# Kernel tuning notes

Measured on AMD Instinct MI355X. Metric: run time of the kernel, lower is better.

The kernel has to match this reference:

```python
import jax, jax.numpy as jnp
import numpy as np

# Dimensions (match input_specs / init_kwargs)
B, T, M, H, E, K = 4, 2048, 1024, 2048, 8, 2
CAP_FACTOR = 1.0  # tutel default capacity_factor
S = B * T
C = int(K * CAP_FACTOR * ((S + E - 1) // E))  # per-expert capacity (tutel Top-k gate)


def setup_inputs() -> dict:
    key = jax.random.key(0)
    ks = jax.random.split(key, 4)
    x = jax.random.normal(ks[0], (B, T, M), jnp.float32)
    wg = jax.random.normal(ks[1], (M, E), jnp.float32) / np.sqrt(M)
    w1 = jax.random.normal(ks[2], (E, M, H), jnp.float32) / np.sqrt(M)
    b1 = jnp.zeros((E, H), jnp.float32)
    w2 = jax.random.normal(ks[3], (E, H, M), jnp.float32) / np.sqrt(H)
    b2 = jnp.zeros((E, M), jnp.float32)
    return {"x": x, "wg": wg, "w1": w1, "b1": b1, "w2": w2, "b2": b2}


def reference(x, wg, w1, b1, w2, b2):
    xf = x.reshape(S, M)
    # ---- Top-k gate (fp32 gate) ----
    logits = xf.astype(jnp.float32) @ wg                 # [S, E]
    scores = jax.nn.softmax(logits, axis=-1)
    topv, topi = jax.lax.top_k(scores, K)                # [S, K]
    gates = topv / (jnp.sum(topv, axis=-1, keepdims=True) + 1e-9)  # normalized top-k gates

    # ---- Dispatch into [E, C, M] buffer with capacity-based token dropping ----
    buf = jnp.zeros((E, C, M), xf.dtype)
    offset = jnp.zeros((E,), jnp.int32)  # tokens already placed per expert (previous slots)
    pos_list, keep_list = [], []
    for j in range(K):  # small fixed loop over top-k slots
        e = topi[:, j]                                   # [S]
        m = jax.nn.one_hot(e, E, dtype=jnp.int32)        # [S, E]
        pos = jnp.sum(jnp.cumsum(m, axis=0) * m, axis=1) - 1 + offset[e]  # position within expert
        offset = offset + jnp.sum(m, axis=0)
        keep = pos < C                                   # drop tokens over capacity
        posc = jnp.minimum(pos, C - 1)
        buf = buf.at[e, posc].add(xf * keep[:, None].astype(xf.dtype))
        pos_list.append(posc)
        keep_list.append(keep)

    # ---- Grouped expert FFN: relu(x W1 + b1) W2 + b2 ----
    h = jax.nn.relu(jnp.einsum('ecm,emh->ech', buf, w1) + b1[:, None, :])  # [E, C, H]
    y = jnp.einsum('ech,ehm->ecm', h, w2) + b2[:, None, :]                 # [E, C, M]

    # ---- Combine with gate weights ----
    out = jnp.zeros_like(xf)
    for j in range(K):
        g = gates[:, j] * keep_list[j].astype(xf.dtype)
        out = out + g[:, None] * y[topi[:, j], pos_list[j]]

    out = out.reshape(B, T, M)
    # result = log_softmax(sum over model_dim, over token dim)
    return jax.nn.log_softmax(jnp.sum(out, axis=2), axis=1)   # [B, T]
```

## Files before the change

### kernel.cpp

```cpp
#include <hip/hip_runtime.h>
#include <hip/hip_bf16.h>
#include <cstdint>
#include <cstddef>

constexpr int Bb = 4;
constexpr int Tt = 2048;
constexpr int Mm = 1024;
constexpr int Hh = 2048;
constexpr int Ee = 8;
constexpr int Ss = Bb * Tt;
constexpr int Cc = 2048;

typedef __attribute__((ext_vector_type(4))) float f32x4;
typedef __attribute__((ext_vector_type(8))) short bf16x8;

__global__ void k_w1t(const float* __restrict__ w1, __hip_bfloat16* __restrict__ w1t) {
    int e = blockIdx.z, m0 = blockIdx.y * 32, h0 = blockIdx.x * 32;
    __shared__ float tile[32][33];
    int t = threadIdx.x;
    const float* src = w1 + (size_t)e * Mm * Hh;
    #pragma unroll
    for (int i = 0; i < 4; i++) {
        int idx = t + i * 256; int r = idx >> 5, c = idx & 31;
        tile[r][c] = src[(size_t)(m0 + r) * Hh + h0 + c];
    }
    __syncthreads();
    __hip_bfloat16* dst = w1t + (size_t)e * Hh * Mm;
    #pragma unroll
    for (int i = 0; i < 4; i++) {
        int idx = t + i * 256; int r = idx >> 5, c = idx & 31;
        dst[(size_t)(h0 + r) * Mm + m0 + c] = __float2bfloat16(tile[c][r]);
    }
}

__global__ void k_w2sum(const float* __restrict__ w2, float* __restrict__ w2sum) {
    int wave = threadIdx.x >> 6, lane = threadIdx.x & 63;
    int r = blockIdx.x * 4 + wave;
    const float4* p = (const float4*)(w2 + (size_t)r * Mm);
    float s = 0.f;
    #pragma unroll
    for (int i = 0; i < 4; i++) { float4 v = p[lane + i * 64]; s += v.x + v.y + v.z + v.w; }
    #pragma unroll
    for (int off = 32; off; off >>= 1) s += __shfl_down(s, off);
    if (lane == 0) w2sum[r] = s;
}

__global__ void k_b2sum(const float* __restrict__ b2, float* __restrict__ b2sum) {
    int e = blockIdx.x; int lane = threadIdx.x;
    const float4* p = (const float4*)(b2 + (size_t)e * Mm);
    float s = 0.f;
    #pragma unroll
    for (int i = 0; i < 4; i++) { float4 v = p[lane + i * 64]; s += v.x + v.y + v.z + v.w; }
    #pragma unroll
    for (int off = 32; off; off >>= 1) s += __shfl_down(s, off);
    if (lane == 0) b2sum[e] = s;
}

__global__ void k_gate(const float* __restrict__ x, const float* __restrict__ wg,
                       int* __restrict__ esel, float* __restrict__ gates) {
    int s = blockIdx.x; int t = threadIdx.x;
    const float4* xr = (const float4*)(x + (size_t)s * Mm);
    float4 xv = xr[t];
    float acc[8];
    #pragma unroll
    for (int e = 0; e < 8; e++) acc[e] = 0.f;
    const float4* wgr = (const float4*)wg;
    #pragma unroll
    for (int k = 0; k < 4; k++) {
        int m = t * 4 + k;
        float xm = (k == 0) ? xv.x : (k == 1) ? xv.y : (k == 2) ? xv.z : xv.w;
        float4 w0 = wgr[m * 2], w1v = wgr[m * 2 + 1];
        acc[0] += xm * w0.x;  acc[1] += xm * w0.y;  acc[2] += xm * w0.z;  acc[3] += xm * w0.w;
        acc[4] += xm * w1v.x; acc[5] += xm * w1v.y; acc[6] += xm * w1v.z; acc[7] += xm * w1v.w;
    }
    #pragma unroll
    for (int off = 32; off; off >>= 1)
        #pragma unroll
        for (int e = 0; e < 8; e++) acc[e] += __shfl_down(acc[e], off);
    __shared__ float red[4][8];
    int wave = t >> 6, lane = t & 63;
    if (lane == 0)
        #pragma unroll
        for (int e = 0; e < 8; e++) red[wave][e] = acc[e];
    __syncthreads();
    if (t == 0) {
        float lg[8];
        #pragma unroll
        for (int e = 0; e < 8; e++) lg[e] = red[0][e] + red[1][e] + red[2][e] + red[3][e];
        float mx = lg[0];
        #pragma unroll
        for (int e = 1; e < 8; e++) mx = fmaxf(mx, lg[e]);
        float ex[8], se = 0.f;
        #pragma unroll
        for (int e = 0; e < 8; e++) { ex[e] = expf(lg[e] - mx); se += ex[e]; }
        float p[8];
        #pragma unroll
        for (int e = 0; e < 8; e++) p[e] = ex[e] / se;
        int i0 = 0; float v0 = p[0];
        #pragma unroll
        for (int e = 1; e < 8; e++) if (p[e] > v0) { v0 = p[e]; i0 = e; }
        int i1 = -1; float v1 = -1.f;
        #pragma unroll
        for (int e = 0; e < 8; e++) if (e != i0 && p[e] > v1) { v1 = p[e]; i1 = e; }
        float den = v0 + v1 + 1e-9f;
        esel[s] = i0; esel[Ss + s] = i1;
        gates[s] = v0 / den; gates[Ss + s] = v1 / den;
    }
}

__global__ void k_pos(const int* __restrict__ esel, int* __restrict__ pos) {
    __shared__ int scan[2][256 * 8];
    __shared__ int offs[8];
    int t = threadIdx.x;
    if (t == 0)
        for (int e = 0; e < 8; e++) offs[e] = 0;
    __syncthreads();
    for (int j = 0; j < 2; j++) {
        int h[8];
        #pragma unroll
        for (int q = 0; q < 8; q++) h[q] = 0;
        int base_s = j * Ss + t * 32;
        for (int i = 0; i < 32; i++) {
            int e = esel[base_s + i];
            #pragma unroll
            for (int q = 0; q < 8; q++) h[q] += (q == e);
        }
        int cur[8];
        #pragma unroll
        for (int q = 0; q < 8; q++) { cur[q] = h[q]; scan[0][t * 8 + q] = h[q]; }
        __syncthreads();
        int sel = 0;
        for (int step = 1; step < 256; step <<= 1) {
            int add[8];
            #pragma unroll
            for (int q = 0; q < 8; q++) add[q] = (t >= step) ? scan[sel][(t - step) * 8 + q] : 0;
            #pragma unroll
            for (int q = 0; q < 8; q++) { cur[q] += add[q]; scan[sel ^ 1][t * 8 + q] = cur[q]; }
            __syncthreads();
            sel ^= 1;
        }
        int total[8];
        #pragma unroll
        for (int q = 0; q < 8; q++) total[q] = scan[sel][255 * 8 + q];
        int cnt[8];
        #pragma unroll
        for (int q = 0; q < 8; q++) cnt[q] = offs[q] + cur[q] - h[q];
        for (int i = 0; i < 32; i++) {
            int e = esel[base_s + i];
            int p = 0;
            #pragma unroll
            for (int q = 0; q < 8; q++) if (q == e) p = cnt[q];
            #pragma unroll
            for (int q = 0; q < 8; q++) cnt[q] += (q == e);
            pos[base_s + i] = p;
        }
        __syncthreads();
        if (t == 0)
            for (int q = 0; q < 8; q++) offs[q] += total[q];
        __syncthreads();
    }
}

__global__ void k_scatter(const float* __restrict__ x, const int* __restrict__ esel,
                          const int* __restrict__ pos, __hip_bfloat16* __restrict__ xbuf) {
    int d = blockIdx.x;
    int p = pos[d];
    if (p >= Cc) return;
    int e = esel[d];
    int s = d & (Ss - 1);
    int t = threadIdx.x;
    const float4* xr = (const float4*)(x + (size_t)s * Mm);
    float4 a = xr[t * 2], b = xr[t * 2 + 1];
    __hip_bfloat16 tmp[8];
    tmp[0] = __float2bfloat16(a.x); tmp[1] = __float2bfloat16(a.y);
    tmp[2] = __float2bfloat16(a.z); tmp[3] = __float2bfloat16(a.w);
    tmp[4] = __float2bfloat16(b.x); tmp[5] = __float2bfloat16(b.y);
    tmp[6] = __float2bfloat16(b.z); tmp[7] = __float2bfloat16(b.w);
    uint4 v;
    __builtin_memcpy(&v, tmp, 16);
    *(uint4*)(xbuf + ((size_t)e * Cc + p) * Mm + t * 8) = v;
}

__global__ __launch_bounds__(256) void k_gemm(
    const __hip_bfloat16* __restrict__ xbuf, const __hip_bfloat16* __restrict__ w1t,
    const float* __restrict__ b1, const float* __restrict__ w2sum,
    float* __restrict__ rowsum) {
    constexpr int LDSS = 40;
    __shared__ __align__(16) __hip_bfloat16 As[128 * LDSS];
    __shared__ __align__(16) __hip_bfloat16 Bs[128 * LDSS];
    int e = blockIdx.z;
    int c0 = blockIdx.y * 128, h0 = blockIdx.x * 128;
    int t = threadIdx.x;
    int wave = t >> 6, lane = t & 63;
    int wm = wave >> 1, wn = wave & 1;
    int r16 = lane & 15, quad = lane >> 4;
    const __hip_bfloat16* Ab = xbuf + (size_t)e * Cc * Mm;
    const __hip_bfloat16* Bb = w1t + (size_t)e * Hh * Mm;
    f32x4 acc[4][4];
    #pragma unroll
    for (int i = 0; i < 4; i++)
        #pragma unroll
        for (int j = 0; j < 4; j++) acc[i][j] = (f32x4){0.f, 0.f, 0.f, 0.f};

    for (int k0 = 0; k0 < Mm; k0 += 32) {
        #pragma unroll
        for (int it = 0; it < 2; ++it) {
            int id2 = t + it * 256; int row = id2 >> 2, q = id2 & 3;
            uint4 va = *(const uint4*)(Ab + (size_t)(c0 + row) * Mm + k0 + q * 8);
            *(uint4*)(As + row * LDSS + q * 8) = va;
            uint4 vb = *(const uint4*)(Bb + (size_t)(h0 + row) * Mm + k0 + q * 8);
            *(uint4*)(Bs + row * LDSS + q * 8) = vb;
        }
        __syncthreads();
        bf16x8 af[4], bfr[4];
        #pragma unroll
        for (int mi = 0; mi < 4; mi++)
            af[mi] = *(const bf16x8*)(As + (wm * 64 + mi * 16 + r16) * LDSS + quad * 8);
        #pragma unroll
        for (int ni = 0; ni < 4; ni++)
            bfr[ni] = *(const bf16x8*)(Bs + (wn * 64 + ni * 16 + r16) * LDSS + quad * 8);
        #pragma unroll
        for (int mi = 0; mi < 4; mi++)
            #pragma unroll
            for (int ni = 0; ni < 4; ni++)
                acc[mi][ni] = __builtin_amdgcn_mfma_f32_16x16x32_bf16(af[mi], bfr[ni], acc[mi][ni], 0, 0, 0);
        __syncthreads();
    }

    float b1v[4], wsv[4];
    #pragma unroll
    for (int ni = 0; ni < 4; ni++) {
        int hg = h0 + wn * 64 + ni * 16 + r16;
        b1v[ni] = b1[e * Hh + hg];
        wsv[ni] = w2sum[e * Hh + hg];
    }
    #pragma unroll
    for (int mi = 0; mi < 4; mi++) {
        #pragma unroll
        for (int r = 0; r < 4; r++) {
            float val = 0.f;
            #pragma unroll
            for (int ni = 0; ni < 4; ni++) {
                float sv = acc[mi][ni][r] + b1v[ni];
                val += fmaxf(sv, 0.f) * wsv[ni];
            }
            #pragma unroll
            for (int off = 1; off < 16; off <<= 1) val += __shfl_xor(val, off);
            if (r16 == 0) {
                int cg = c0 + wm * 64 + mi * 16 + quad * 4 + r;
                atomicAdd(&rowsum[e * Cc + cg], val);
            }
        }
    }
}

__global__ __launch_bounds__(1024) void k_final(
    const int* __restrict__ esel, const int* __restrict__ pos,
    const float* __restrict__ gates, const float* __restrict__ rowsum,
    const float* __restrict__ b2sum, float* __restrict__ out) {
    int b = blockIdx.x; int t = threadIdx.x;
    __shared__ float red[1024];
    float vv[2];
    #pragma unroll
    for (int i = 0; i < 2; i++) {
        int tok = t + i * 1024;
        int s = b * Tt + tok;
        float acc = 0.f;
        #pragma unroll
        for (int j = 0; j < 2; j++) {
            int d = j * Ss + s;
            int p = pos[d];
            if (p < Cc) {
                int e = esel[d];
                acc += gates[d] * (rowsum[e * Cc + p] + b2sum[e]);
            }
        }
        vv[i] = acc;
    }
    float m = fmaxf(vv[0], vv[1]);
    red[t] = m; __syncthreads();
    for (int st = 512; st; st >>= 1) { if (t < st) red[t] = fmaxf(red[t], red[t + st]); __syncthreads(); }
    float mx = red[0];
    __syncthreads();
    float se = expf(vv[0] - mx) + expf(vv[1] - mx);
    red[t] = se; __syncthreads();
    for (int st = 512; st; st >>= 1) { if (t < st) red[t] += red[t + st]; __syncthreads(); }
    float lse = logf(red[0]);
    #pragma unroll
    for (int i = 0; i < 2; i++) {
        int tok = t + i * 1024;
        out[b * Tt + tok] = vv[i] - mx - lse;
    }
}

extern "C" void kernel_launch(void* const* d_in, const int* in_sizes, int n_in,
                              void* d_out, int out_size, void* d_ws, size_t ws_size,
                              hipStream_t stream) {
    const float* x  = (const float*)d_in[0];
    const float* wg = (const float*)d_in[1];
    const float* w1 = (const float*)d_in[2];
    const float* b1 = (const float*)d_in[3];
    const float* w2 = (const float*)d_in[4];
    const float* b2 = (const float*)d_in[5];
    float* out = (float*)d_out;

    char* ws = (char*)d_ws;
    size_t off = 0;
    auto alloc = [&](size_t bytes) -> void* {
        void* p = ws + off;
        off += (bytes + 255) & ~(size_t)255;
        return p;
    };
    float* w2sum  = (float*)alloc((size_t)Ee * Hh * 4);
    float* b2sum  = (float*)alloc(Ee * 4);
    int*   esel   = (int*)alloc((size_t)2 * Ss * 4);
    int*   pos    = (int*)alloc((size_t)2 * Ss * 4);
    float* gates  = (float*)alloc((size_t)2 * Ss * 4);
    float* rowsum = (float*)alloc((size_t)Ee * Cc * 4);
    __hip_bfloat16* w1t  = (__hip_bfloat16*)alloc((size_t)Ee * Hh * Mm * 2);
    __hip_bfloat16* xbuf = (__hip_bfloat16*)alloc((size_t)Ee * Cc * Mm * 2);

    hipMemsetAsync(rowsum, 0, (size_t)Ee * Cc * 4, stream);
    k_w1t<<<dim3(Hh / 32, Mm / 32, Ee), 256, 0, stream>>>(w1, w1t);
    k_w2sum<<<Ee * Hh / 4, 256, 0, stream>>>(w2, w2sum);
    k_b2sum<<<Ee, 64, 0, stream>>>(b2, b2sum);
    k_gate<<<Ss, 256, 0, stream>>>(x, wg, esel, gates);
    k_pos<<<1, 256, 0, stream>>>(esel, pos);
    k_scatter<<<2 * Ss, 128, 0, stream>>>(x, esel, pos, xbuf);
    k_gemm<<<dim3(Hh / 128, Cc / 128, Ee), 256, 0, stream>>>(xbuf, w1t, b1, w2sum, rowsum);
    k_final<<<Bb, 1024, 0, stream>>>(esel, pos, gates, rowsum, b2sum, out);
}
```

Baseline: 355.3 us.

## Rework transpose, gate, position scan, and GEMM loads across the MoE pipeline

The weight transpose now uses 64x64 tiles with vectorized float4 reads and 16-byte bf16 writes. The gate kernel handles one token per wave instead of one per block, which removes the LDS reduction. The single-block serial position scan is replaced by a parallel ballot/popcount rank plus a small per-expert block-prefix kernel, and final positions are now computed inside the scatter kernel. The GEMM loads tiles straight to LDS with global_load_lds, drops the LDS padding (which risks bank conflicts), and swizzles block order for L2 locality.

```diff
diff --git a/kernel.cpp b/kernel.cpp
--- a/kernel.cpp
+++ b/kernel.cpp
@@ -14,22 +14,37 @@
 typedef __attribute__((ext_vector_type(4))) float f32x4;
 typedef __attribute__((ext_vector_type(8))) short bf16x8;
 
-__global__ void k_w1t(const float* __restrict__ w1, __hip_bfloat16* __restrict__ w1t) {
-    int e = blockIdx.z, m0 = blockIdx.y * 32, h0 = blockIdx.x * 32;
-    __shared__ float tile[32][33];
+__device__ inline void load_lds16(const void* g, void* l) {
+    __builtin_amdgcn_global_load_lds(
+        (const __attribute__((address_space(1))) unsigned int*)g,
+        (__attribute__((address_space(3))) unsigned int*)l, 16, 0, 0);
+}
+
+__global__ __launch_bounds__(256) void k_w1t(const float* __restrict__ w1,
+                                             __hip_bfloat16* __restrict__ w1t) {
+    __shared__ float tile[64][65];
+    int e = blockIdx.z, m0 = blockIdx.y * 64, h0 = blockIdx.x * 64;
     int t = threadIdx.x;
     const float* src = w1 + (size_t)e * Mm * Hh;
     #pragma unroll
     for (int i = 0; i < 4; i++) {
-        int idx = t + i * 256; int r = idx >> 5, c = idx & 31;
-        tile[r][c] = src[(size_t)(m0 + r) * Hh + h0 + c];
+        int idx = t + i * 256;
+        int r = idx >> 4, c4 = idx & 15;
+        float4 v = *(const float4*)(src + (size_t)(m0 + r) * Hh + h0 + c4 * 4);
+        tile[r][c4 * 4 + 0] = v.x; tile[r][c4 * 4 + 1] = v.y;
+        tile[r][c4 * 4 + 2] = v.z; tile[r][c4 * 4 + 3] = v.w;
     }
     __syncthreads();
     __hip_bfloat16* dst = w1t + (size_t)e * Hh * Mm;
     #pragma unroll
-    for (int i = 0; i < 4; i++) {
-        int idx = t + i * 256; int r = idx >> 5, c = idx & 31;
-        dst[(size_t)(h0 + r) * Mm + m0 + c] = __float2bfloat16(tile[c][r]);
+    for (int i = 0; i < 2; i++) {
+        int idx = t + i * 256;
+        int r = idx >> 3, c8 = idx & 7;
+        __hip_bfloat16 tmp[8];
+        #pragma unroll
+        for (int k = 0; k < 8; k++) tmp[k] = __float2bfloat16(tile[c8 * 8 + k][r]);
+        uint4 vv; __builtin_memcpy(&vv, tmp, 16);
+        *(uint4*)(dst + (size_t)(h0 + r) * Mm + m0 + c8 * 8) = vv;
     }
 }
 
@@ -56,46 +71,43 @@
     if (lane == 0) b2sum[e] = s;
 }
 
-__global__ void k_gate(const float* __restrict__ x, const float* __restrict__ wg,
-                       int* __restrict__ esel, float* __restrict__ gates) {
-    int s = blockIdx.x; int t = threadIdx.x;
+__global__ __launch_bounds__(256) void k_gate(const float* __restrict__ x,
+                                              const float* __restrict__ wg,
+                                              int* __restrict__ esel, float* __restrict__ gates) {
+    int s = (blockIdx.x * 256 + threadIdx.x) >> 6;
+    int lane = threadIdx.x & 63;
     const float4* xr = (const float4*)(x + (size_t)s * Mm);
-    float4 xv = xr[t];
+    const float4* wgr = (const float4*)wg;
     float acc[8];
     #pragma unroll
     for (int e = 0; e < 8; e++) acc[e] = 0.f;
-    const float4* wgr = (const float4*)wg;
-    #pragma unroll
-    for (int k = 0; k < 4; k++) {
-        int m = t * 4 + k;
-        float xm = (k == 0) ? xv.x : (k == 1) ? xv.y : (k == 2) ? xv.z : xv.w;
-        float4 w0 = wgr[m * 2], w1v = wgr[m * 2 + 1];
-        acc[0] += xm * w0.x;  acc[1] += xm * w0.y;  acc[2] += xm * w0.z;  acc[3] += xm * w0.w;
-        acc[4] += xm * w1v.x; acc[5] += xm * w1v.y; acc[6] += xm * w1v.z; acc[7] += xm * w1v.w;
+    #pragma unroll
+    for (int i = 0; i < 4; i++) {
+        float4 xv = xr[lane + i * 64];
+        int mbase = (lane + i * 64) * 4;
+        #pragma unroll
+        for (int k = 0; k < 4; k++) {
+            int m = mbase + k;
+            float xm = (k == 0) ? xv.x : (k == 1) ? xv.y : (k == 2) ? xv.z : xv.w;
+            float4 w0 = wgr[m * 2], w1v = wgr[m * 2 + 1];
+            acc[0] += xm * w0.x;  acc[1] += xm * w0.y;  acc[2] += xm * w0.z;  acc[3] += xm * w0.w;
+            acc[4] += xm * w1v.x; acc[5] += xm * w1v.y; acc[6] += xm * w1v.z; acc[7] += xm * w1v.w;
+        }
     }
     #pragma unroll
     for (int off = 32; off; off >>= 1)
         #pragma unroll
         for (int e = 0; e < 8; e++) acc[e] += __shfl_down(acc[e], off);
-    __shared__ float red[4][8];
-    int wave = t >> 6, lane = t & 63;
-    if (lane == 0)
-        #pragma unroll
-        for (int e = 0; e < 8; e++) red[wave][e] = acc[e];
-    __syncthreads();
-    if (t == 0) {
-        float lg[8];
-        #pragma unroll
-        for (int e = 0; e < 8; e++) lg[e] = red[0][e] + red[1][e] + red[2][e] + red[3][e];
-        float mx = lg[0];
-        #pragma unroll
-        for (int e = 1; e < 8; e++) mx = fmaxf(mx, lg[e]);
-        float ex[8], se = 0.f;
-        #pragma unroll
-        for (int e = 0; e < 8; e++) { ex[e] = expf(lg[e] - mx); se += ex[e]; }
-        float p[8];
-        #pragma unroll
-        for (int e = 0; e < 8; e++) p[e] = ex[e] / se;
+    if (lane == 0) {
+        float mx = acc[0];
+        #pragma unroll
+        for (int e = 1; e < 8; e++) mx = fmaxf(mx, acc[e]);
+        float p[8], se = 0.f;
+        #pragma unroll
+        for (int e = 0; e < 8; e++) { p[e] = expf(acc[e] - mx); se += p[e]; }
+        float inv = 1.f / se;
+        #pragma unroll
+        for (int e = 0; e < 8; e++) p[e] *= inv;
         int i0 = 0; float v0 = p[0];
         #pragma unroll
         for (int e = 1; e < 8; e++) if (p[e] > v0) { v0 = p[e]; i0 = e; }
@@ -108,65 +120,55 @@
     }
 }
 
-__global__ void k_pos(const int* __restrict__ esel, int* __restrict__ pos) {
-    __shared__ int scan[2][256 * 8];
-    __shared__ int offs[8];
-    int t = threadIdx.x;
-    if (t == 0)
-        for (int e = 0; e < 8; e++) offs[e] = 0;
+__global__ __launch_bounds__(256) void k_posA(const int* __restrict__ esel,
+                                              int* __restrict__ lrank, int* __restrict__ blockhist) {
+    int b = blockIdx.x, t = threadIdx.x;
+    int d = b * 256 + t;
+    int e = esel[d];
+    int wave = t >> 6, lane = t & 63;
+    __shared__ int wh[4][8];
+    unsigned long long mymask = 0;
+    #pragma unroll
+    for (int q = 0; q < 8; q++) {
+        unsigned long long m = __ballot(e == q);
+        if (q == e) mymask = m;
+        if (lane == 0) wh[wave][q] = (int)__popcll(m);
+    }
     __syncthreads();
-    for (int j = 0; j < 2; j++) {
-        int h[8];
-        #pragma unroll
-        for (int q = 0; q < 8; q++) h[q] = 0;
-        int base_s = j * Ss + t * 32;
-        for (int i = 0; i < 32; i++) {
-            int e = esel[base_s + i];
-            #pragma unroll
-            for (int q = 0; q < 8; q++) h[q] += (q == e);
-        }
-        int cur[8];
-        #pragma unroll
-        for (int q = 0; q < 8; q++) { cur[q] = h[q]; scan[0][t * 8 + q] = h[q]; }
-        __syncthreads();
-        int sel = 0;
-        for (int step = 1; step < 256; step <<= 1) {
-            int add[8];
-            #pragma unroll
-            for (int q = 0; q < 8; q++) add[q] = (t >= step) ? scan[sel][(t - step) * 8 + q] : 0;
-            #pragma unroll
-            for (int q = 0; q < 8; q++) { cur[q] += add[q]; scan[sel ^ 1][t * 8 + q] = cur[q]; }
-            __syncthreads();
-            sel ^= 1;
-        }
-        int total[8];
-        #pragma unroll
-        for (int q = 0; q < 8; q++) total[q] = scan[sel][255 * 8 + q];
-        int cnt[8];
-        #pragma unroll
-        for (int q = 0; q < 8; q++) cnt[q] = offs[q] + cur[q] - h[q];
-        for (int i = 0; i < 32; i++) {
-            int e = esel[base_s + i];
-            int p = 0;
-            #pragma unroll
-            for (int q = 0; q < 8; q++) if (q == e) p = cnt[q];
-            #pragma unroll
-            for (int q = 0; q < 8; q++) cnt[q] += (q == e);
-            pos[base_s + i] = p;
-        }
-        __syncthreads();
-        if (t == 0)
-            for (int q = 0; q < 8; q++) offs[q] += total[q];
-        __syncthreads();
-    }
-}
-
-__global__ void k_scatter(const float* __restrict__ x, const int* __restrict__ esel,
-                          const int* __restrict__ pos, __hip_bfloat16* __restrict__ xbuf) {
+    int prefix = (int)__popcll(mymask & ((1ull << lane) - 1ull));
+    for (int w = 0; w < wave; w++) prefix += wh[w][e];
+    lrank[d] = prefix;
+    if (t < 8) blockhist[b * 8 + t] = wh[0][t] + wh[1][t] + wh[2][t] + wh[3][t];
+}
+
+__global__ void k_posB(const int* __restrict__ blockhist, int* __restrict__ blockbase) {
+    int q = threadIdx.x;
+    if (q < 8) {
+        int run = 0;
+        for (int b = 0; b < 64; b++) {
+            blockbase[b * 8 + q] = run;
+            run += blockhist[b * 8 + q];
+        }
+    }
+}
+
+__global__ __launch_bounds__(128) void k_scatter(const float* __restrict__ x,
+                                                 const int* __restrict__ esel,
+                                                 const int* __restrict__ lrank,
+                                                 const int* __restrict__ blockbase,
+                                                 int* __restrict__ pos,
+                                                 __hip_bfloat16* __restrict__ xbuf) {
     int d = blockIdx.x;
-    int p = pos[d];
+    __shared__ int sp, se;
+    if (threadIdx.x == 0) {
+        int e = esel[d];
+        int p = blockbase[(d >> 8) * 8 + e] + lrank[d];
+        pos[d] = p; sp = p; se = e;
+    }
+    __syncthreads();
+    int p = sp;
     if (p >= Cc) return;
-    int e = esel[d];
+    int e = se;
     int s = d & (Ss - 1);
     int t = threadIdx.x;
     const float4* xr = (const float4*)(x + (size_t)s * Mm);
@@ -185,17 +187,20 @@
     const __hip_bfloat16* __restrict__ xbuf, const __hip_bfloat16* __restrict__ w1t,
     const float* __restrict__ b1, const float* __restrict__ w2sum,
     float* __restrict__ rowsum) {
-    constexpr int LDSS = 40;
-    __shared__ __align__(16) __hip_bfloat16 As[128 * LDSS];
-    __shared__ __align__(16) __hip_bfloat16 Bs[128 * LDSS];
-    int e = blockIdx.z;
-    int c0 = blockIdx.y * 128, h0 = blockIdx.x * 128;
+    __shared__ __align__(16) __hip_bfloat16 As[128 * 32];
+    __shared__ __align__(16) __hip_bfloat16 Bs[128 * 32];
+    int e = blockIdx.y;
+    int bid = blockIdx.x;
+    int sq = bid >> 4, in16 = bid & 15;
+    int hb = (sq & 3) * 4 + (in16 & 3);
+    int cb = (sq >> 2) * 4 + (in16 >> 2);
+    int c0 = cb * 128, h0 = hb * 128;
     int t = threadIdx.x;
     int wave = t >> 6, lane = t & 63;
     int wm = wave >> 1, wn = wave & 1;
     int r16 = lane & 15, quad = lane >> 4;
     const __hip_bfloat16* Ab = xbuf + (size_t)e * Cc * Mm;
-    const __hip_bfloat16* Bb = w1t + (size_t)e * Hh * Mm;
+    const __hip_bfloat16* Bp = w1t + (size_t)e * Hh * Mm;
     f32x4 acc[4][4];
     #pragma unroll
     for (int i = 0; i < 4; i++)
@@ -204,21 +209,20 @@
 
     for (int k0 = 0; k0 < Mm; k0 += 32) {
         #pragma unroll
-        for (int it = 0; it < 2; ++it) {
-            int id2 = t + it * 256; int row = id2 >> 2, q = id2 & 3;
-            uint4 va = *(const uint4*)(Ab + (size_t)(c0 + row) * Mm + k0 + q * 8);
-            *(uint4*)(As + row * LDSS + q * 8) = va;
-            uint4 vb = *(const uint4*)(Bb + (size_t)(h0 + row) * Mm + k0 + q * 8);
-            *(uint4*)(Bs + row * LDSS + q * 8) = vb;
+        for (int p = 0; p < 2; ++p) {
+            int ci = t + p * 256;
+            int row = ci >> 2, q = ci & 3;
+            load_lds16(Ab + (size_t)(c0 + row) * Mm + k0 + q * 8, As + ci * 8);
+            load_lds16(Bp + (size_t)(h0 + row) * Mm + k0 + q * 8, Bs + ci * 8);
         }
         __syncthreads();
         bf16x8 af[4], bfr[4];
         #pragma unroll
         for (int mi = 0; mi < 4; mi++)
-            af[mi] = *(const bf16x8*)(As + (wm * 64 + mi * 16 + r16) * LDSS + quad * 8);
+            af[mi] = *(const bf16x8*)(As + (wm * 64 + mi * 16 + r16) * 32 + quad * 8);
         #pragma unroll
         for (int ni = 0; ni < 4; ni++)
-            bfr[ni] = *(const bf16x8*)(Bs + (wn * 64 + ni * 16 + r16) * LDSS + quad * 8);
+            bfr[ni] = *(const bf16x8*)(Bs + (wn * 64 + ni * 16 + r16) * 32 + quad * 8);
         #pragma unroll
         for (int mi = 0; mi < 4; mi++)
             #pragma unroll
@@ -311,22 +315,26 @@
         off += (bytes + 255) & ~(size_t)255;
         return p;
     };
-    float* w2sum  = (float*)alloc((size_t)Ee * Hh * 4);
-    float* b2sum  = (float*)alloc(Ee * 4);
-    int*   esel   = (int*)alloc((size_t)2 * Ss * 4);
-    int*   pos    = (int*)alloc((size_t)2 * Ss * 4);
-    float* gates  = (float*)alloc((size_t)2 * Ss * 4);
-    float* rowsum = (float*)alloc((size_t)Ee * Cc * 4);
+    float* w2sum    = (float*)alloc((size_t)Ee * Hh * 4);
+    float* b2sum    = (float*)alloc(Ee * 4);
+    int*   esel     = (int*)alloc((size_t)2 * Ss * 4);
+    int*   lrank    = (int*)alloc((size_t)2 * Ss * 4);
+    int*   blockhist= (int*)alloc((size_t)64 * 8 * 4);
+    int*   blockbase= (int*)alloc((size_t)64 * 8 * 4);
+    int*   pos      = (int*)alloc((size_t)2 * Ss * 4);
+    float* gates    = (float*)alloc((size_t)2 * Ss * 4);
+    float* rowsum   = (float*)alloc((size_t)Ee * Cc * 4);
     __hip_bfloat16* w1t  = (__hip_bfloat16*)alloc((size_t)Ee * Hh * Mm * 2);
     __hip_bfloat16* xbuf = (__hip_bfloat16*)alloc((size_t)Ee * Cc * Mm * 2);
 
     hipMemsetAsync(rowsum, 0, (size_t)Ee * Cc * 4, stream);
-    k_w1t<<<dim3(Hh / 32, Mm / 32, Ee), 256, 0, stream>>>(w1, w1t);
+    k_w1t<<<dim3(Hh / 64, Mm / 64, Ee), 256, 0, stream>>>(w1, w1t);
     k_w2sum<<<Ee * Hh / 4, 256, 0, stream>>>(w2, w2sum);
     k_b2sum<<<Ee, 64, 0, stream>>>(b2, b2sum);
-    k_gate<<<Ss, 256, 0, stream>>>(x, wg, esel, gates);
-    k_pos<<<1, 256, 0, stream>>>(esel, pos);
-    k_scatter<<<2 * Ss, 128, 0, stream>>>(x, esel, pos, xbuf);
-    k_gemm<<<dim3(Hh / 128, Cc / 128, Ee), 256, 0, stream>>>(xbuf, w1t, b1, w2sum, rowsum);
+    k_gate<<<Ss / 4, 256, 0, stream>>>(x, wg, esel, gates);
+    k_posA<<<64, 256, 0, stream>>>(esel, lrank, blockhist);
+    k_posB<<<1, 64, 0, stream>>>(blockhist, blockbase);
+    k_scatter<<<2 * Ss, 128, 0, stream>>>(x, esel, lrank, blockbase, pos, xbuf);
+    k_gemm<<<dim3(16 * 16, Ee), 256, 0, stream>>>(xbuf, w1t, b1, w2sum, rowsum);
     k_final<<<Bb, 1024, 0, stream>>>(esel, pos, gates, rowsum, b2sum, out);
 }
```

Measured after the change: 323.8 us. 8.9% less time.
